# Performance work log

Measured on AMD Instinct MI355X. Metric: run time of the kernel, lower is better.

Reference implementation:

```python
import jax, jax.numpy as jnp
import numpy as np

ALPHA = 0.2       # LeakyReLU negative slope
MASK_FILL = 1e-15 # value placed at non-edges before softmax (as in the original)
OUT_DIM = 64


def setup_inputs() -> dict:
    key = jax.random.key(0)
    k1, k2, k3, k4 = jax.random.split(key, 4)
    N, IN_DIM, D = 8192, 256, OUT_DIM
    h = jax.random.normal(k1, (N, IN_DIM), dtype=jnp.float32)
    # dense 0/1 adjacency (float, used only via A > 0)
    A = jax.random.randint(k2, (N, N), 0, 2).astype(jnp.float32)
    W = jax.random.normal(k3, (IN_DIM, D), dtype=jnp.float32) * (1.0 / np.sqrt(IN_DIM))
    a = jax.random.normal(k4, (2 * D,), dtype=jnp.float32) * (1.0 / np.sqrt(2 * D))
    return {"h": h, "A": A, "W": W, "a": a}


def reference(h, A, W, a):
    D = OUT_DIM
    Wh = h @ W                                   # [N, D]
    # attn([Wh_i || Wh_j]) == Wh_i . a[:D] + Wh_j . a[D:]  -- fused, avoids [N,N,2D]
    s_src = Wh @ a[:D]                           # [N]
    s_dst = Wh @ a[D:]                           # [N]
    e = jax.nn.leaky_relu(s_src[:, None] + s_dst[None, :], negative_slope=ALPHA)  # [N, N]
    attention = jnp.where(A > 0, e, MASK_FILL)
    attention = jax.nn.softmax(attention, axis=1)
    h_prime = attention @ Wh                     # [N, D]
    return jax.nn.elu(h_prime)                   # concat=True branch
```

## Files before the change

kernel.cpp:

```cpp
#include <hip/hip_runtime.h>
#include <hip/hip_bf16.h>

#define GAT_N 8192
#define GAT_K 256
#define GAT_D 64
#define GAT_ALPHA 0.2f
#define GAT_FILL 1e-15f

typedef float f32x4 __attribute__((ext_vector_type(4)));
typedef short bf16x8 __attribute__((ext_vector_type(8)));

static __device__ __forceinline__ unsigned f2bf_u(float x) {
  unsigned u = __float_as_uint(x);
  u += 0x7FFFu + ((u >> 16) & 1u);
  return u >> 16;
}

static __device__ __forceinline__ float rfl(float x) {
  return __uint_as_float(__builtin_amdgcn_readfirstlane(__float_as_uint(x)));
}

__global__ __launch_bounds__(256) void k_prep(const float* __restrict__ h,
                                              const float* __restrict__ W,
                                              const float* __restrict__ av,
                                              float* __restrict__ s_src,
                                              float* __restrict__ s_dst,
                                              short* __restrict__ WhT,
                                              float* __restrict__ bmax) {
  __shared__ short T[4][64][8];
  __shared__ float wmLds[4];
  const int tid = threadIdx.x;
  const int wv = tid >> 6, lane = tid & 63;
  const int r0 = blockIdx.x * 32 + wv * 8;

  float acc[8], acc2[8];
#pragma unroll
  for (int r = 0; r < 8; ++r) { acc[r] = 0.f; acc2[r] = 0.f; }

  for (int kc = 0; kc < GAT_K; kc += 32) {
    float Wreg[32];
#pragma unroll
    for (int e = 0; e < 32; ++e) Wreg[e] = W[(size_t)(kc + e) * GAT_D + lane];
#pragma unroll
    for (int r = 0; r < 8; ++r) {
      const f32x4* h4 = (const f32x4*)(h + (size_t)(r0 + r) * GAT_K + kc);
#pragma unroll
      for (int q = 0; q < 8; ++q) {
        f32x4 hv = h4[q];
        acc[r] += hv[0] * Wreg[4 * q + 0];
        acc2[r] += hv[1] * Wreg[4 * q + 1];
        acc[r] += hv[2] * Wreg[4 * q + 2];
        acc2[r] += hv[3] * Wreg[4 * q + 3];
      }
    }
  }

  const float a_s = av[lane];
  const float a_d = av[64 + lane];
  float wmax = -3.0e38f;
#pragma unroll
  for (int r = 0; r < 8; ++r) {
    const float accf = acc[r] + acc2[r];
    T[wv][lane][r] = (short)f2bf_u(accf);
    float vs = accf * a_s, vd = accf * a_d;
#pragma unroll
    for (int off = 32; off > 0; off >>= 1) {
      vs += __shfl_xor(vs, off);
      vd += __shfl_xor(vd, off);
    }
    if (lane == 0) { s_src[r0 + r] = vs; s_dst[r0 + r] = vd; }
    wmax = fmaxf(wmax, vd);
  }
  bf16x8 vt = *(const bf16x8*)&T[wv][lane][0];
  *(bf16x8*)(WhT + (size_t)lane * GAT_N + r0) = vt;

  if (lane == 0) wmLds[wv] = wmax;
  __syncthreads();
  if (tid == 0) {
    bmax[blockIdx.x] = fmaxf(fmaxf(wmLds[0], wmLds[1]), fmaxf(wmLds[2], wmLds[3]));
  }
}

#define BM 16
#define JB 1024
#define NCHUNK (GAT_N / JB)
#define NWAVE 8

__global__ __launch_bounds__(512, 4) void k_attn(
    const float* __restrict__ A,
    const float* __restrict__ s_src,
    const float* __restrict__ s_dst,
    const short* __restrict__ WhT,
    const float* __restrict__ bmax,
    float* __restrict__ out) {
  __shared__ char smem[65536];

  const int tid = threadIdx.x;
  const int wv = tid >> 6, lane = tid & 63;
  const int rsub = lane & 15, kg = lane >> 4;
  const int i0 = blockIdx.x * BM;
  const int par = wv >> 2;
  const int cth = tid & 255;

  float bm = fmaxf(fmaxf(bmax[lane], bmax[lane + 64]),
                   fmaxf(bmax[lane + 128], bmax[lane + 192]));
#pragma unroll
  for (int off = 32; off > 0; off >>= 1) bm = fmaxf(bm, __shfl_xor(bm, off));
  const float tmax = bm;

  float F1_[8], F2_[8], ns_[8], c_[8];
#pragma unroll
  for (int s = 0; s < 8; ++s) {
    float sc = s_src[i0 + 2 * s + par];
    float x0 = sc + tmax;
    float m = fmaxf(fmaxf(x0, GAT_ALPHA * x0), GAT_FILL);
    F1_[s] = rfl(__expf(sc - m));
    F2_[s] = rfl(__expf(GAT_ALPHA * sc - m));
    ns_[s] = rfl(-sc);
    c_[s] = rfl(__expf(GAT_FILL - m));
  }

  bf16x8 ones;
#pragma unroll
  for (int e = 0; e < 8; ++e) ones[e] = (short)0x3F80;

  f32x4 acc0 = {0.f, 0.f, 0.f, 0.f};
  f32x4 acc1 = {0.f, 0.f, 0.f, 0.f};
  f32x4 acc2 = {0.f, 0.f, 0.f, 0.f};
  f32x4 acc3 = {0.f, 0.f, 0.f, 0.f};
  f32x4 accl = {0.f, 0.f, 0.f, 0.f};

  const short* pb0 = WhT + (size_t)(0 * 16 + rsub) * GAT_N;
  const short* pb1 = WhT + (size_t)(1 * 16 + rsub) * GAT_N;
  const short* pb2 = WhT + (size_t)(2 * 16 + rsub) * GAT_N;
  const short* pb3 = WhT + (size_t)(3 * 16 + rsub) * GAT_N;

  const float* Abase = A + (size_t)(i0 + par) * GAT_N + cth * 4;
  auto aaddr = [&](int g) {
    return Abase + (size_t)((g & 7) * 2) * GAT_N + (size_t)(g >> 3) * JB;
  };

  f32x4 buf[4];
#pragma unroll
  for (int g = 0; g < 4; ++g) buf[g] = *(const f32x4*)aaddr(g);

  for (int chunk = 0; chunk < NCHUNK; ++chunk) {
    const int jc = chunk * JB;
    const int tile = (chunk & 1) << 15;
    const f32x4 t = *(const f32x4*)(s_dst + jc + cth * 4);

    f32x4 E1, E2;
#pragma unroll
    for (int e = 0; e < 4; ++e) {
      E1[e] = __expf(t[e]);
      E2[e] = __expf(GAT_ALPHA * t[e]);
    }

#pragma unroll
    for (int s = 0; s < 8; ++s) {
      const int g = chunk * 8 + s;
      f32x4 av = buf[g & 3];
      if (g + 4 < 64) buf[(g + 4) & 3] = *(const f32x4*)aaddr(g + 4);
      const float F1 = F1_[s], F2 = F2_[s], negs = ns_[s], cc = c_[s];
      float p[4];
#pragma unroll
      for (int e = 0; e < 4; ++e) {
        float m1 = E1[e] * F1;
        float m2 = E2[e] * F2;
        float psel = (t[e] >= negs) ? m1 : m2;
        p[e] = (av[e] > 0.f) ? psel : cc;
      }
      __hip_bfloat162 pa = __float22bfloat162_rn(float2{p[0], p[1]});
      __hip_bfloat162 pb = __float22bfloat162_rn(float2{p[2], p[3]});
      uint2 w;
      __builtin_memcpy(&w.x, &pa, 4);
      __builtin_memcpy(&w.y, &pb, 4);
      const int row = 2 * s + par;
      *(uint2*)(&smem[tile + (row << 11) + (((cth << 3)) ^ ((row & 7) << 4))]) = w;
    }
    __syncthreads();

#pragma unroll
    for (int kq = 0; kq < 4; ++kq) {
      const int cbyte = (wv << 8) + (kq << 6) + (kg << 4);
      bf16x8 af = *(const bf16x8*)(&smem[tile + (rsub << 11) + (cbyte ^ ((rsub & 7) << 4))]);
      const int bcol = jc + (wv << 7) + (kq << 5) + (kg << 3);
      bf16x8 b0 = *(const bf16x8*)(pb0 + bcol);
      bf16x8 b1 = *(const bf16x8*)(pb1 + bcol);
      bf16x8 b2 = *(const bf16x8*)(pb2 + bcol);
      bf16x8 b3 = *(const bf16x8*)(pb3 + bcol);
      acc0 = __builtin_amdgcn_mfma_f32_16x16x32_bf16(af, b0, acc0, 0, 0, 0);
      acc1 = __builtin_amdgcn_mfma_f32_16x16x32_bf16(af, b1, acc1, 0, 0, 0);
      acc2 = __builtin_amdgcn_mfma_f32_16x16x32_bf16(af, b2, acc2, 0, 0, 0);
      acc3 = __builtin_amdgcn_mfma_f32_16x16x32_bf16(af, b3, acc3, 0, 0, 0);
      accl = __builtin_amdgcn_mfma_f32_16x16x32_bf16(af, ones, accl, 0, 0, 0);
    }
  }

  __syncthreads();

  float* lds_o = (float*)smem;
  float* lds_l = (float*)(smem + 32768);
#pragma unroll
  for (int r = 0; r < 4; ++r) {
    const int orow = kg * 4 + r;
    lds_o[wv * 1024 + orow * 64 + 0 * 16 + rsub] = acc0[r];
    lds_o[wv * 1024 + orow * 64 + 1 * 16 + rsub] = acc1[r];
    lds_o[wv * 1024 + orow * 64 + 2 * 16 + rsub] = acc2[r];
    lds_o[wv * 1024 + orow * 64 + 3 * 16 + rsub] = acc3[r];
    if (rsub == 0) lds_l[wv * 16 + orow] = accl[r];
  }
  __syncthreads();

  for (int idx = tid; idx < BM * GAT_D; idx += 512) {
    const int r = idx >> 6, c = idx & 63;
    float o = 0.f, ll = 0.f;
#pragma unroll
    for (int w = 0; w < NWAVE; ++w) {
      o += lds_o[w * 1024 + r * 64 + c];
      ll += lds_l[w * 16 + r];
    }
    float val = o / ll;
    out[(size_t)(i0 + r) * GAT_D + c] = (val > 0.f) ? val : (__expf(val) - 1.f);
  }
}

extern "C" void kernel_launch(void* const* d_in, const int* in_sizes, int n_in,
                              void* d_out, int out_size, void* d_ws, size_t ws_size,
                              hipStream_t stream) {
  const float* h = (const float*)d_in[0];
  const float* A = (const float*)d_in[1];
  const float* W = (const float*)d_in[2];
  const float* a = (const float*)d_in[3];
  float* out = (float*)d_out;

  const size_t need = 69632 + (size_t)GAT_D * GAT_N * 2;
  if (ws_size < need) return;
  float* bmax = (float*)d_ws;
  float* s_src = (float*)((char*)d_ws + 4096);
  float* s_dst = (float*)((char*)d_ws + 36864);
  short* WhT = (short*)((char*)d_ws + 69632);

  k_prep<<<dim3(256), dim3(256), 0, stream>>>(h, W, a, s_src, s_dst, WhT, bmax);
  k_attn<<<dim3(GAT_N / BM), dim3(512), 0, stream>>>(A, s_src, s_dst, WhT, bmax, out);
}
```

Baseline: 131.4 us.

## Split attention columns across two blocks with per-wave LDS tiles and a combine kernel

Each row block is now split into two halves of the column range, doubling the grid, and partial numerators and denominators are written to workspace. A new combine kernel sums the halves, normalizes and applies ELU. Each wave now owns a private LDS tile, which removes the per-chunk __syncthreads, and LDS shrinks to allow 8 waves per SIMD in the launch bounds. Probabilities are computed with a single exp of max(t+e1, alpha*t+e2) instead of two precomputed exponent products and a select. The costs are more exp work per element, an extra launch, and extra global traffic for the partials.

```diff
diff --git a/kernel.cpp b/kernel.cpp
--- a/kernel.cpp
+++ b/kernel.cpp
@@ -14,10 +14,6 @@
   unsigned u = __float_as_uint(x);
   u += 0x7FFFu + ((u >> 16) & 1u);
   return u >> 16;
-}
-
-static __device__ __forceinline__ float rfl(float x) {
-  return __uint_as_float(__builtin_amdgcn_readfirstlane(__float_as_uint(x)));
 }
 
 __global__ __launch_bounds__(256) void k_prep(const float* __restrict__ h,
@@ -82,25 +78,27 @@
 }
 
 #define BM 16
-#define JB 1024
-#define NCHUNK (GAT_N / JB)
 #define NWAVE 8
 
-__global__ __launch_bounds__(512, 4) void k_attn(
+__global__ __launch_bounds__(512, 8) void k_attn(
     const float* __restrict__ A,
     const float* __restrict__ s_src,
     const float* __restrict__ s_dst,
     const short* __restrict__ WhT,
     const float* __restrict__ bmax,
-    float* __restrict__ out) {
-  __shared__ char smem[65536];
+    float* __restrict__ o_part,
+    float* __restrict__ l_part) {
+  __shared__ char smem[33536];
 
   const int tid = threadIdx.x;
   const int wv = tid >> 6, lane = tid & 63;
+  const int hi = lane >> 5, l5 = lane & 31;
   const int rsub = lane & 15, kg = lane >> 4;
-  const int i0 = blockIdx.x * BM;
-  const int par = wv >> 2;
-  const int cth = tid & 255;
+  const int ib = blockIdx.x >> 1, jh = blockIdx.x & 1;
+  const int i0 = ib * BM;
+  const int wvbase = wv << 12;
+
+  float* scon = (float*)(smem + 33280);
 
   float bm = fmaxf(fmaxf(bmax[lane], bmax[lane + 64]),
                    fmaxf(bmax[lane + 128], bmax[lane + 192]));
@@ -108,17 +106,15 @@
   for (int off = 32; off > 0; off >>= 1) bm = fmaxf(bm, __shfl_xor(bm, off));
   const float tmax = bm;
 
-  float F1_[8], F2_[8], ns_[8], c_[8];
-#pragma unroll
-  for (int s = 0; s < 8; ++s) {
-    float sc = s_src[i0 + 2 * s + par];
+  if (tid < BM) {
+    float sc = s_src[i0 + tid];
     float x0 = sc + tmax;
     float m = fmaxf(fmaxf(x0, GAT_ALPHA * x0), GAT_FILL);
-    F1_[s] = rfl(__expf(sc - m));
-    F2_[s] = rfl(__expf(GAT_ALPHA * sc - m));
-    ns_[s] = rfl(-sc);
-    c_[s] = rfl(__expf(GAT_FILL - m));
-  }
+    scon[tid] = sc - m;
+    scon[16 + tid] = GAT_ALPHA * sc - m;
+    scon[32 + tid] = __expf(GAT_FILL - m);
+  }
+  __syncthreads();
 
   bf16x8 ones;
 #pragma unroll
@@ -135,56 +131,46 @@
   const short* pb2 = WhT + (size_t)(2 * 16 + rsub) * GAT_N;
   const short* pb3 = WhT + (size_t)(3 * 16 + rsub) * GAT_N;
 
-  const float* Abase = A + (size_t)(i0 + par) * GAT_N + cth * 4;
+  const float* Abase = A + (size_t)(i0 + hi) * GAT_N + jh * 4096 + wv * 128 + l5 * 4;
   auto aaddr = [&](int g) {
-    return Abase + (size_t)((g & 7) * 2) * GAT_N + (size_t)(g >> 3) * JB;
+    return Abase + (size_t)((g & 7) * 2) * GAT_N + (size_t)(g >> 3) * 1024;
   };
 
-  f32x4 buf[4];
-#pragma unroll
-  for (int g = 0; g < 4; ++g) buf[g] = *(const f32x4*)aaddr(g);
-
-  for (int chunk = 0; chunk < NCHUNK; ++chunk) {
-    const int jc = chunk * JB;
-    const int tile = (chunk & 1) << 15;
-    const f32x4 t = *(const f32x4*)(s_dst + jc + cth * 4);
-
-    f32x4 E1, E2;
-#pragma unroll
-    for (int e = 0; e < 4; ++e) {
-      E1[e] = __expf(t[e]);
-      E2[e] = __expf(GAT_ALPHA * t[e]);
-    }
+  f32x4 buf[2];
+  buf[0] = *(const f32x4*)aaddr(0);
+  buf[1] = *(const f32x4*)aaddr(1);
+
+  for (int c = 0; c < 4; ++c) {
+    const int jb = jh * 4096 + c * 1024 + wv * 128;
+    const f32x4 t = *(const f32x4*)(s_dst + jb + l5 * 4);
 
 #pragma unroll
     for (int s = 0; s < 8; ++s) {
-      const int g = chunk * 8 + s;
-      f32x4 av = buf[g & 3];
-      if (g + 4 < 64) buf[(g + 4) & 3] = *(const f32x4*)aaddr(g + 4);
-      const float F1 = F1_[s], F2 = F2_[s], negs = ns_[s], cc = c_[s];
+      const int g = c * 8 + s;
+      f32x4 av = buf[g & 1];
+      if (g + 2 < 32) buf[g & 1] = *(const f32x4*)aaddr(g + 2);
+      const int row = 2 * s + hi;
+      const float e1 = scon[row], e2 = scon[16 + row], cc = scon[32 + row];
       float p[4];
 #pragma unroll
       for (int e = 0; e < 4; ++e) {
-        float m1 = E1[e] * F1;
-        float m2 = E2[e] * F2;
-        float psel = (t[e] >= negs) ? m1 : m2;
-        p[e] = (av[e] > 0.f) ? psel : cc;
+        float arg = fmaxf(t[e] + e1, fmaf(GAT_ALPHA, t[e], e2));
+        float pe = __expf(arg);
+        p[e] = (av[e] > 0.f) ? pe : cc;
       }
       __hip_bfloat162 pa = __float22bfloat162_rn(float2{p[0], p[1]});
       __hip_bfloat162 pb = __float22bfloat162_rn(float2{p[2], p[3]});
       uint2 w;
       __builtin_memcpy(&w.x, &pa, 4);
       __builtin_memcpy(&w.y, &pb, 4);
-      const int row = 2 * s + par;
-      *(uint2*)(&smem[tile + (row << 11) + (((cth << 3)) ^ ((row & 7) << 4))]) = w;
-    }
-    __syncthreads();
+      *(uint2*)(&smem[wvbase + (row << 8) + ((l5 << 3) ^ ((row & 7) << 4))]) = w;
+    }
 
 #pragma unroll
     for (int kq = 0; kq < 4; ++kq) {
-      const int cbyte = (wv << 8) + (kq << 6) + (kg << 4);
-      bf16x8 af = *(const bf16x8*)(&smem[tile + (rsub << 11) + (cbyte ^ ((rsub & 7) << 4))]);
-      const int bcol = jc + (wv << 7) + (kq << 5) + (kg << 3);
+      const int raddr = wvbase + (rsub << 8) + (((kq << 6) | (kg << 4)) ^ ((rsub & 7) << 4));
+      bf16x8 af = *(const bf16x8*)(&smem[raddr]);
+      const int bcol = jb + (kq << 5) + (kg << 3);
       bf16x8 b0 = *(const bf16x8*)(pb0 + bcol);
       bf16x8 b1 = *(const bf16x8*)(pb1 + bcol);
       bf16x8 b2 = *(const bf16x8*)(pb2 + bcol);
@@ -213,16 +199,33 @@
   __syncthreads();
 
   for (int idx = tid; idx < BM * GAT_D; idx += 512) {
-    const int r = idx >> 6, c = idx & 63;
+    const int r = idx >> 6, cc = idx & 63;
     float o = 0.f, ll = 0.f;
 #pragma unroll
     for (int w = 0; w < NWAVE; ++w) {
-      o += lds_o[w * 1024 + r * 64 + c];
+      o += lds_o[w * 1024 + r * 64 + cc];
       ll += lds_l[w * 16 + r];
     }
-    float val = o / ll;
-    out[(size_t)(i0 + r) * GAT_D + c] = (val > 0.f) ? val : (__expf(val) - 1.f);
-  }
+    o_part[((size_t)jh * GAT_N + i0 + r) * GAT_D + cc] = o;
+    if (cc == 0) l_part[jh * GAT_N + i0 + r] = ll;
+  }
+}
+
+__global__ __launch_bounds__(256) void k_comb(const float* __restrict__ o_part,
+                                              const float* __restrict__ l_part,
+                                              float* __restrict__ out) {
+  const int idx = blockIdx.x * 256 + threadIdx.x;
+  const int row = idx >> 4;
+  f32x4 o0 = *(const f32x4*)(o_part + (size_t)idx * 4);
+  f32x4 o1 = *(const f32x4*)(o_part + (size_t)GAT_N * GAT_D + (size_t)idx * 4);
+  const float l = l_part[row] + l_part[GAT_N + row];
+  f32x4 v;
+#pragma unroll
+  for (int e = 0; e < 4; ++e) {
+    float val = (o0[e] + o1[e]) / l;
+    v[e] = (val > 0.f) ? val : (__expf(val) - 1.f);
+  }
+  *(f32x4*)(out + (size_t)idx * 4) = v;
 }
 
 extern "C" void kernel_launch(void* const* d_in, const int* in_sizes, int n_in,
@@ -234,13 +237,17 @@
   const float* a = (const float*)d_in[3];
   float* out = (float*)d_out;
 
-  const size_t need = 69632 + (size_t)GAT_D * GAT_N * 2;
+  const size_t need = 5373952 + 65536;
   if (ws_size < need) return;
   float* bmax = (float*)d_ws;
   float* s_src = (float*)((char*)d_ws + 4096);
   float* s_dst = (float*)((char*)d_ws + 36864);
   short* WhT = (short*)((char*)d_ws + 69632);
+  float* o_part = (float*)((char*)d_ws + 1179648);
+  float* l_part = (float*)((char*)d_ws + 5373952);
 
   k_prep<<<dim3(256), dim3(256), 0, stream>>>(h, W, a, s_src, s_dst, WhT, bmax);
-  k_attn<<<dim3(GAT_N / BM), dim3(512), 0, stream>>>(A, s_src, s_dst, WhT, bmax, out);
-}
+  k_attn<<<dim3(2 * GAT_N / BM), dim3(512), 0, stream>>>(A, s_src, s_dst, WhT,
+                                                         bmax, o_part, l_part);
+  k_comb<<<dim3(GAT_N * GAT_D / 1024), dim3(256), 0, stream>>>(o_part, l_part, out);
+}
```

New measurement: 159.0 us. +21.0%, slower.

## Give each wave a private LDS tile and prefetch A and WhT into registers

Applied to the files above, without the earlier changes.

Each wave now owns a 128-column slice of every 512-column chunk. It writes its bf16 probability tile into its own LDS region and reads it back without any block-wide barrier inside the main loop. The next chunk's A values, s_dst values and WhT B-fragments are loaded into registers one iteration ahead, so global latency overlaps the exp and MFMA work. The block drops to 256 threads with 16 KB of LDS. This trades the old double-buffered shared tile and its per-chunk __syncthreads for higher register pressure.

```diff
diff --git a/kernel.cpp b/kernel.cpp
--- a/kernel.cpp
+++ b/kernel.cpp
@@ -14,10 +14,6 @@
   unsigned u = __float_as_uint(x);
   u += 0x7FFFu + ((u >> 16) & 1u);
   return u >> 16;
-}
-
-static __device__ __forceinline__ float rfl(float x) {
-  return __uint_as_float(__builtin_amdgcn_readfirstlane(__float_as_uint(x)));
 }
 
 __global__ __launch_bounds__(256) void k_prep(const float* __restrict__ h,
@@ -82,25 +78,22 @@
 }
 
 #define BM 16
-#define JB 1024
-#define NCHUNK (GAT_N / JB)
-#define NWAVE 8
-
-__global__ __launch_bounds__(512, 4) void k_attn(
+
+__global__ __launch_bounds__(256, 2) void k_attn(
     const float* __restrict__ A,
     const float* __restrict__ s_src,
     const float* __restrict__ s_dst,
     const short* __restrict__ WhT,
     const float* __restrict__ bmax,
     float* __restrict__ out) {
-  __shared__ char smem[65536];
+  __shared__ char smem[16640];
 
   const int tid = threadIdx.x;
   const int wv = tid >> 6, lane = tid & 63;
+  const int hi = lane >> 5, l5 = lane & 31;
   const int rsub = lane & 15, kg = lane >> 4;
   const int i0 = blockIdx.x * BM;
-  const int par = wv >> 2;
-  const int cth = tid & 255;
+  const int wvbase = wv << 12;
 
   float bm = fmaxf(fmaxf(bmax[lane], bmax[lane + 64]),
                    fmaxf(bmax[lane + 128], bmax[lane + 192]));
@@ -108,16 +101,17 @@
   for (int off = 32; off > 0; off >>= 1) bm = fmaxf(bm, __shfl_xor(bm, off));
   const float tmax = bm;
 
-  float F1_[8], F2_[8], ns_[8], c_[8];
+  float F1_[8], F2_[8], ns_[8], cc_[8];
 #pragma unroll
   for (int s = 0; s < 8; ++s) {
-    float sc = s_src[i0 + 2 * s + par];
+    const int row = 2 * s + hi;
+    float sc = s_src[i0 + row];
     float x0 = sc + tmax;
     float m = fmaxf(fmaxf(x0, GAT_ALPHA * x0), GAT_FILL);
-    F1_[s] = rfl(__expf(sc - m));
-    F2_[s] = rfl(__expf(GAT_ALPHA * sc - m));
-    ns_[s] = rfl(-sc);
-    c_[s] = rfl(__expf(GAT_FILL - m));
+    F1_[s] = __expf(sc - m);
+    F2_[s] = __expf(GAT_ALPHA * sc - m);
+    ns_[s] = -sc;
+    cc_[s] = __expf(GAT_FILL - m);
   }
 
   bf16x8 ones;
@@ -130,77 +124,84 @@
   f32x4 acc3 = {0.f, 0.f, 0.f, 0.f};
   f32x4 accl = {0.f, 0.f, 0.f, 0.f};
 
-  const short* pb0 = WhT + (size_t)(0 * 16 + rsub) * GAT_N;
-  const short* pb1 = WhT + (size_t)(1 * 16 + rsub) * GAT_N;
-  const short* pb2 = WhT + (size_t)(2 * 16 + rsub) * GAT_N;
-  const short* pb3 = WhT + (size_t)(3 * 16 + rsub) * GAT_N;
-
-  const float* Abase = A + (size_t)(i0 + par) * GAT_N + cth * 4;
-  auto aaddr = [&](int g) {
-    return Abase + (size_t)((g & 7) * 2) * GAT_N + (size_t)(g >> 3) * JB;
-  };
-
-  f32x4 buf[4];
-#pragma unroll
-  for (int g = 0; g < 4; ++g) buf[g] = *(const f32x4*)aaddr(g);
-
-  for (int chunk = 0; chunk < NCHUNK; ++chunk) {
-    const int jc = chunk * JB;
-    const int tile = (chunk & 1) << 15;
-    const f32x4 t = *(const f32x4*)(s_dst + jc + cth * 4);
+  const int colbase = wv * 128;
+  const float* Abase = A + (size_t)(i0 + hi) * GAT_N + colbase + l5 * 4;
+  const short* pb0 = WhT + (size_t)(0 * 16 + rsub) * GAT_N + colbase + (kg << 3);
+  const short* pb1 = WhT + (size_t)(1 * 16 + rsub) * GAT_N + colbase + (kg << 3);
+  const short* pb2 = WhT + (size_t)(2 * 16 + rsub) * GAT_N + colbase + (kg << 3);
+  const short* pb3 = WhT + (size_t)(3 * 16 + rsub) * GAT_N + colbase + (kg << 3);
+  const float* tbase = s_dst + colbase + l5 * 4;
+
+  f32x4 Ar[8];
+#pragma unroll
+  for (int s = 0; s < 8; ++s)
+    Ar[s] = *(const f32x4*)(Abase + (size_t)(2 * s) * GAT_N);
+  bf16x8 bq0[4], bq1[4], bq2[4], bq3[4];
+#pragma unroll
+  for (int kq = 0; kq < 4; ++kq) {
+    bq0[kq] = *(const bf16x8*)(pb0 + (kq << 5));
+    bq1[kq] = *(const bf16x8*)(pb1 + (kq << 5));
+    bq2[kq] = *(const bf16x8*)(pb2 + (kq << 5));
+    bq3[kq] = *(const bf16x8*)(pb3 + (kq << 5));
+  }
+  f32x4 tcur = *(const f32x4*)tbase;
+
+  for (int c = 0; c < 16; ++c) {
+    const int jc = c * 512;
+    const int jn = (c < 15) ? jc + 512 : jc;
+
+    f32x4 tnxt = *(const f32x4*)(tbase + jn);
 
     f32x4 E1, E2;
 #pragma unroll
     for (int e = 0; e < 4; ++e) {
-      E1[e] = __expf(t[e]);
-      E2[e] = __expf(GAT_ALPHA * t[e]);
+      E1[e] = __expf(tcur[e]);
+      E2[e] = __expf(GAT_ALPHA * tcur[e]);
     }
 
 #pragma unroll
     for (int s = 0; s < 8; ++s) {
-      const int g = chunk * 8 + s;
-      f32x4 av = buf[g & 3];
-      if (g + 4 < 64) buf[(g + 4) & 3] = *(const f32x4*)aaddr(g + 4);
-      const float F1 = F1_[s], F2 = F2_[s], negs = ns_[s], cc = c_[s];
+      f32x4 av = Ar[s];
+      Ar[s] = *(const f32x4*)(Abase + (size_t)(2 * s) * GAT_N + jn);
       float p[4];
 #pragma unroll
       for (int e = 0; e < 4; ++e) {
-        float m1 = E1[e] * F1;
-        float m2 = E2[e] * F2;
-        float psel = (t[e] >= negs) ? m1 : m2;
-        p[e] = (av[e] > 0.f) ? psel : cc;
+        float m1 = E1[e] * F1_[s];
+        float m2 = E2[e] * F2_[s];
+        float psel = (tcur[e] >= ns_[s]) ? m1 : m2;
+        p[e] = (av[e] > 0.f) ? psel : cc_[s];
       }
       __hip_bfloat162 pa = __float22bfloat162_rn(float2{p[0], p[1]});
       __hip_bfloat162 pb = __float22bfloat162_rn(float2{p[2], p[3]});
       uint2 w;
       __builtin_memcpy(&w.x, &pa, 4);
       __builtin_memcpy(&w.y, &pb, 4);
-      const int row = 2 * s + par;
-      *(uint2*)(&smem[tile + (row << 11) + (((cth << 3)) ^ ((row & 7) << 4))]) = w;
-    }
-    __syncthreads();
+      const int row = 2 * s + hi;
+      *(uint2*)(&smem[wvbase + (row << 8) + ((l5 << 3) ^ ((row & 7) << 4))]) = w;
+    }
 
 #pragma unroll
     for (int kq = 0; kq < 4; ++kq) {
-      const int cbyte = (wv << 8) + (kq << 6) + (kg << 4);
-      bf16x8 af = *(const bf16x8*)(&smem[tile + (rsub << 11) + (cbyte ^ ((rsub & 7) << 4))]);
-      const int bcol = jc + (wv << 7) + (kq << 5) + (kg << 3);
-      bf16x8 b0 = *(const bf16x8*)(pb0 + bcol);
-      bf16x8 b1 = *(const bf16x8*)(pb1 + bcol);
-      bf16x8 b2 = *(const bf16x8*)(pb2 + bcol);
-      bf16x8 b3 = *(const bf16x8*)(pb3 + bcol);
-      acc0 = __builtin_amdgcn_mfma_f32_16x16x32_bf16(af, b0, acc0, 0, 0, 0);
-      acc1 = __builtin_amdgcn_mfma_f32_16x16x32_bf16(af, b1, acc1, 0, 0, 0);
-      acc2 = __builtin_amdgcn_mfma_f32_16x16x32_bf16(af, b2, acc2, 0, 0, 0);
-      acc3 = __builtin_amdgcn_mfma_f32_16x16x32_bf16(af, b3, acc3, 0, 0, 0);
+      const int raddr =
+          wvbase + (rsub << 8) + (((kq << 6) | (kg << 4)) ^ ((rsub & 7) << 4));
+      bf16x8 af = *(const bf16x8*)(&smem[raddr]);
+      acc0 = __builtin_amdgcn_mfma_f32_16x16x32_bf16(af, bq0[kq], acc0, 0, 0, 0);
+      acc1 = __builtin_amdgcn_mfma_f32_16x16x32_bf16(af, bq1[kq], acc1, 0, 0, 0);
+      acc2 = __builtin_amdgcn_mfma_f32_16x16x32_bf16(af, bq2[kq], acc2, 0, 0, 0);
+      acc3 = __builtin_amdgcn_mfma_f32_16x16x32_bf16(af, bq3[kq], acc3, 0, 0, 0);
       accl = __builtin_amdgcn_mfma_f32_16x16x32_bf16(af, ones, accl, 0, 0, 0);
-    }
+      bq0[kq] = *(const bf16x8*)(pb0 + jn + (kq << 5));
+      bq1[kq] = *(const bf16x8*)(pb1 + jn + (kq << 5));
+      bq2[kq] = *(const bf16x8*)(pb2 + jn + (kq << 5));
+      bq3[kq] = *(const bf16x8*)(pb3 + jn + (kq << 5));
+    }
+    tcur = tnxt;
   }
 
   __syncthreads();
 
   float* lds_o = (float*)smem;
-  float* lds_l = (float*)(smem + 32768);
+  float* lds_l = (float*)(smem + 16384);
 #pragma unroll
   for (int r = 0; r < 4; ++r) {
     const int orow = kg * 4 + r;
@@ -212,16 +213,16 @@
   }
   __syncthreads();
 
-  for (int idx = tid; idx < BM * GAT_D; idx += 512) {
-    const int r = idx >> 6, c = idx & 63;
+  for (int idx = tid; idx < BM * GAT_D; idx += 256) {
+    const int r = idx >> 6, col = idx & 63;
     float o = 0.f, ll = 0.f;
 #pragma unroll
-    for (int w = 0; w < NWAVE; ++w) {
-      o += lds_o[w * 1024 + r * 64 + c];
+    for (int w = 0; w < 4; ++w) {
+      o += lds_o[w * 1024 + r * 64 + col];
       ll += lds_l[w * 16 + r];
     }
     float val = o / ll;
-    out[(size_t)(i0 + r) * GAT_D + c] = (val > 0.f) ? val : (__expf(val) - 1.f);
+    out[(size_t)(i0 + r) * GAT_D + col] = (val > 0.f) ? val : (__expf(val) - 1.f);
   }
 }
 
@@ -242,5 +243,5 @@
   short* WhT = (short*)((char*)d_ws + 69632);
 
   k_prep<<<dim3(256), dim3(256), 0, stream>>>(h, W, a, s_src, s_dst, WhT, bmax);
-  k_attn<<<dim3(GAT_N / BM), dim3(512), 0, stream>>>(A, s_src, s_dst, WhT, bmax, out);
-}
+  k_attn<<<dim3(GAT_N / BM), dim3(256), 0, stream>>>(A, s_src, s_dst, WhT, bmax, out);
+}
```

Measured after the change: 125.7 us. -4.3%, faster.
